# Performance work log

Hardware: AMD Instinct MI355X
Metric: run time of the kernel (lower is better)

The kernel has to match this reference:

```python
import jax, jax.numpy as jnp
import numpy as np

B, C, H, W = 64, 2048, 14, 14
HID, OUT = 2048, 256
NUM_HEADS = 8
SCALE = 1.0
BN_EPS = 1e-5
NORM_EPS = 1e-12


def setup_inputs() -> dict:
    key = jax.random.key(0)
    ks = jax.random.split(key, 5)
    inp = {
        "x": jax.random.normal(ks[0], (B, C, H, W), dtype=jnp.float32),
        # proj MLP1D: conv1(k=1) -> BN -> ReLU -> conv2(k=1), bias=False
        "w1_p": jax.random.normal(ks[1], (HID, C), dtype=jnp.float32) * 0.02,
        "g_p": jnp.ones((HID,), dtype=jnp.float32),
        "b_p": jnp.zeros((HID,), dtype=jnp.float32),
        "w2_p": jax.random.normal(ks[2], (OUT, HID), dtype=jnp.float32) * 0.02,
        # proj_obj MLP1D (same structure)
        "w1_o": jax.random.normal(ks[3], (HID, C), dtype=jnp.float32) * 0.02,
        "g_o": jnp.ones((HID,), dtype=jnp.float32),
        "b_o": jnp.zeros((HID,), dtype=jnp.float32),
        "w2_o": jax.random.normal(ks[4], (OUT, HID), dtype=jnp.float32) * 0.02,
    }
    return inp


def _mlp1d(x, w1, gamma, beta, w2):
    # x: [b, c_in, L]; 1x1 conv == channel matmul
    h = jnp.einsum('oc,bcl->bol', w1, x)  # [b, HID, L]
    # BatchNorm1d, training mode: stats over (batch, length) per channel
    mu = jnp.mean(h, axis=(0, 2), keepdims=True)
    var = jnp.mean(jnp.square(h - mu), axis=(0, 2), keepdims=True)
    h = (h - mu) * jax.lax.rsqrt(var + BN_EPS)
    h = h * gamma[None, :, None] + beta[None, :, None]
    h = jax.nn.relu(h)
    return jnp.einsum('oc,bcl->bol', w2, h)  # [b, OUT, L]


def reference(x, w1_p, g_p, b_p, w2_p, w1_o, g_o, b_o, w2_o):
    b, c, h, w = x.shape
    L = h * w
    xf = x.reshape(b, c, L)                       # [b, c, L]
    x_pool = jnp.mean(xf, axis=2, keepdims=True)  # adaptive_avg_pool2d(1)
    z = _mlp1d(jnp.concatenate([x_pool, xf], axis=2), w1_p, g_p, b_p, w2_p)  # [b, OUT, L+1]
    z_g = z[:, :, :1]          # [b, OUT, 1]
    z_feat = z[:, :, 1:]       # [b, OUT, L]
    # L2 normalize over channel dim, then scale
    nrm = jnp.sqrt(jnp.sum(jnp.square(z_feat), axis=1, keepdims=True))
    a = z_feat / jnp.maximum(nrm, NORM_EPS) / SCALE
    a = a.reshape(b, NUM_HEADS, -1, L)            # [b, H, K, L], K = OUT/H
    obj_attn_raw = jax.nn.softmax(a, axis=-1)
    obj_attn = obj_attn_raw                        # group branch: same softmax
    xh = xf.reshape(b, NUM_HEADS, c // NUM_HEADS, L)
    # matmul(x, attn^T): [b,H,Ch,L] x [b,H,K,L] -> [b,H,Ch,K]
    obj_val = jnp.einsum('bhcl,bhkl->bhck', xh, obj_attn)
    obj_val = obj_val.reshape(b, c, obj_attn.shape[2])  # [b, c, K]
    obj_val = _mlp1d(obj_val, w1_o, g_o, b_o, w2_o)      # [b, OUT, K]
    return (z_g, obj_val, obj_attn, obj_attn_raw)
```

## Files before the change

kernel.cpp:

```cpp
#include <hip/hip_runtime.h>
#include <hip/hip_bf16.h>
#include <math.h>

typedef __bf16 bf16;
typedef bf16 bf16x8 __attribute__((ext_vector_type(8)));
typedef float f32x4 __attribute__((ext_vector_type(4)));

constexpr int BATCH = 64;
constexpr int CIN   = 2048;
constexpr int HIDN  = 2048;
constexpr int OUTN  = 256;
constexpr int LL    = 196;
constexpr int LCAT  = 197;
constexpr int P1V   = BATCH * LCAT;
constexpr int P1P   = 12672;
constexpr size_t O_ZG   = 0;
constexpr size_t O_OVAL = (size_t)BATCH * OUTN;
constexpr size_t O_ATT  = O_OVAL + (size_t)BATCH * OUTN * 32;
constexpr size_t O_ATTR = O_ATT + (size_t)BATCH * OUTN * LL;

constexpr size_t WS_XCAT = 0;
constexpr size_t WS_V2   = WS_XCAT;
constexpr size_t WS_H2T  = WS_XCAT + (size_t)(16u<<20);
constexpr size_t WS_PART = WS_XCAT + (size_t)(28u<<20);
constexpr size_t WS_HT   = 51904512;
constexpr size_t WS_Z    = WS_HT + 51904512;
constexpr size_t WS_W1B  = WS_Z + 12976128;
constexpr size_t WS_W2B  = WS_W1B + 8388608;
constexpr size_t WS_W1OB = WS_W2B + 1048576;
constexpr size_t WS_W2OB = WS_W1OB + 8388608;
constexpr size_t WS_NRM  = WS_W2OB + 1048576;
constexpr size_t WS_SC1  = WS_NRM + 50176;
constexpr size_t WS_SH1  = WS_SC1 + 8192;
constexpr size_t WS_SC2  = WS_SH1 + 8192;
constexpr size_t WS_SH2  = WS_SC2 + 8192;

__device__ __forceinline__ void gload16(const bf16* g, bf16* l){
  __builtin_amdgcn_global_load_lds((const __attribute__((address_space(1))) void*)g,
                                   (__attribute__((address_space(3))) void*)l, 16, 0, 0);
}

__global__ __launch_bounds__(256) void cast_k(const float* __restrict__ s, bf16* __restrict__ d, int n){
  int i = blockIdx.x * 256 + threadIdx.x;
  if (i < n) d[i] = (bf16)s[i];
}
__global__ __launch_bounds__(256) void zero_b16(bf16* p, int n){
  int i = blockIdx.x * 256 + threadIdx.x;
  if (i < n) p[i] = (bf16)0.f;
}

__global__ __launch_bounds__(256) void prep_k(const float* __restrict__ x, bf16* __restrict__ xcat){
  __shared__ float xs[64][201];
  int b  = blockIdx.x >> 5;
  int cg = blockIdx.x & 31;
  int c0 = cg * 64;
  int t  = threadIdx.x;
  const float* xb = x + ((size_t)b * CIN + c0) * LL;
  #pragma unroll
  for (int i = 0; i < 16; i++){
    int idx = i * 256 + t;
    int cc = idx >> 6, q = idx & 63;
    if (q < 49){
      float4 v = *(const float4*)(xb + (size_t)cc * LL + q * 4);
      xs[cc][q*4+0] = v.x; xs[cc][q*4+1] = v.y; xs[cc][q*4+2] = v.z; xs[cc][q*4+3] = v.w;
    }
  }
  __syncthreads();
  if (t < 64){
    float s = 0.f;
    for (int l = 0; l < LL; l++) s += xs[t][l];
    xcat[(size_t)(b * LCAT) * CIN + c0 + t] = (bf16)(s * (1.f / (float)LL));
  }
  int lw = t >> 3, cg8 = t & 7;
  #pragma unroll
  for (int pass = 0; pass < 7; pass++){
    int l = pass * 32 + lw;
    if (l < LL){
      bf16x8 w;
      #pragma unroll
      for (int j = 0; j < 8; j++) w[j] = (bf16)xs[cg8 * 8 + j][l];
      *(bf16x8*)(xcat + (size_t)(b * LCAT + 1 + l) * CIN + c0 + cg8 * 8) = w;
    }
  }
}

__global__ __launch_bounds__(256) void stats_part_k(const bf16* __restrict__ src, int rows, int rpg,
                                                    float* __restrict__ part){
  int o  = threadIdx.x * 8;
  int r0 = blockIdx.x * rpg;
  int r1 = min(rows, r0 + rpg);
  float s[8] = {0.f,0.f,0.f,0.f,0.f,0.f,0.f,0.f};
  float q[8] = {0.f,0.f,0.f,0.f,0.f,0.f,0.f,0.f};
  for (int r = r0; r < r1; r++){
    bf16x8 v = *(const bf16x8*)(src + (size_t)r * 2048 + o);
    #pragma unroll
    for (int j = 0; j < 8; j++){ float f = (float)v[j]; s[j] += f; q[j] += f * f; }
  }
  float* p = part + (size_t)blockIdx.x * 4096;
  #pragma unroll
  for (int j = 0; j < 8; j++){ p[o + j] = s[j]; p[2048 + o + j] = q[j]; }
}

__global__ __launch_bounds__(256) void finalize_k(const float* __restrict__ part, int np,
                                                  const float* __restrict__ g, const float* __restrict__ b,
                                                  float n, float* __restrict__ scale, float* __restrict__ shift){
  int o = blockIdx.x * 256 + threadIdx.x;
  float s = 0.f, q = 0.f;
  for (int p = 0; p < np; p++){
    s += part[(size_t)p * 4096 + o];
    q += part[(size_t)p * 4096 + 2048 + o];
  }
  float mu  = s / n;
  float var = q / n - mu * mu;
  float sc  = g[o] / sqrtf(var + 1e-5f);
  scale[o] = sc;
  shift[o] = b[o] - mu * sc;
}

__global__ __launch_bounds__(256) void zg_k(const float* __restrict__ z, float* __restrict__ dout){
  int gidx = blockIdx.x * 256 + threadIdx.x;
  int b = gidx >> 8, c = gidx & 255;
  dout[O_ZG + gidx] = z[(size_t)c * P1P + b * LCAT];
}

__global__ __launch_bounds__(256) void nrm_k(const float* __restrict__ z, float* __restrict__ nrm){
  int b = blockIdx.x, t = threadIdx.x;
  if (t >= LL) return;
  float acc = 0.f;
  const float* zb = z + (size_t)b * LCAT + 1 + t;
  for (int c = 0; c < OUTN; c++){
    float v = zb[(size_t)c * P1P];
    acc += v * v;
  }
  nrm[b * LL + t] = sqrtf(acc);
}

__global__ __launch_bounds__(64) void softmax_k(const float* __restrict__ z, const float* __restrict__ nrm,
                                                float* __restrict__ dout){
  int bc = blockIdx.x;
  int b  = bc >> 8;
  int lane = threadIdx.x;
  const float* zr = z + (size_t)(bc & 255) * P1P + b * LCAT + 1;
  const float* nr = nrm + b * LL;
  float a[4];
  float mx = -1e30f;
  #pragma unroll
  for (int j = 0; j < 4; j++){
    int l = lane + j * 64;
    if (l < LL){
      float v = zr[l] / fmaxf(nr[l], 1e-12f);
      a[j] = v; mx = fmaxf(mx, v);
    } else a[j] = -1e30f;
  }
  #pragma unroll
  for (int s = 1; s < 64; s <<= 1) mx = fmaxf(mx, __shfl_xor(mx, s, 64));
  float sum = 0.f;
  #pragma unroll
  for (int j = 0; j < 4; j++){
    a[j] = (a[j] > -1e29f) ? expf(a[j] - mx) : 0.f;
    sum += a[j];
  }
  #pragma unroll
  for (int s = 1; s < 64; s <<= 1) sum += __shfl_xor(sum, s, 64);
  float inv = 1.f / sum;
  float* o1 = dout + O_ATT  + (size_t)bc * LL;
  float* o2 = dout + O_ATTR + (size_t)bc * LL;
  #pragma unroll
  for (int j = 0; j < 4; j++){
    int l = lane + j * 64;
    if (l < LL){ float r = a[j] * inv; o1[l] = r; o2[l] = r; }
  }
}

template<int CFG>
__global__ __launch_bounds__(256)
void gemm_k(const void* __restrict__ Ap, const void* __restrict__ Qp, void* __restrict__ Cp,
            const float* __restrict__ sc, const float* __restrict__ sh)
{
  constexpr int BM  = (CFG==5) ? 32 : (CFG==4 ? 64 : 128);
  constexpr int BN  = (CFG==5) ? 256 : (CFG==4 ? 64 : 128);
  constexpr int WR  = (CFG==5) ? 1 : 2;
  constexpr int WC  = 4 / WR;
  constexpr int WTM = BM / WR, WTN = BN / WC;
  constexpr int FM  = WTM / 16, FN = WTN / 16;
  constexpr int KT  = (CFG==5) ? 4 : 32;
  constexpr bool F32S = (CFG==5);
  constexpr bool QBN  = (CFG==2) || (CFG==4);
  constexpr bool AGL  = !F32S;
  constexpr bool QGL  = (CFG==1) || (CFG==3);
  constexpr int LDA = F32S ? LL : 2048;
  constexpr int LDQ = F32S ? LL : 2048;
  constexpr int CA  = BM / 32;
  constexpr int CQ  = BN / 32;

  __shared__ bf16 Ps[BM * 64];
  __shared__ bf16 Qs[BN * 64];

  const int t = threadIdx.x;
  const int lane = t & 63;
  const int wid  = t >> 6;
  const int wr = wid / WC, wc = wid % WC;
  const int sw8 = ((lane & 7) ^ (lane >> 3)) * 8;

  size_t aBase = 0, qBase = 0;
  int mOff = 0, nOff = 0;
  if constexpr (CFG == 5){
    int bh = blockIdx.x;
    aBase = (size_t)bh * 32 * LL;
    qBase = ((size_t)(bh >> 3) * 2048 + (size_t)(bh & 7) * 256) * LL;
    mOff = (bh >> 3) * 32;
    nOff = (bh & 7) * 256;
  } else if constexpr (CFG == 1){
    int bid = blockIdx.x;
    int wg = (bid & 7) * 198 + (bid >> 3);
    mOff = (wg >> 4) * BM;  nOff = (wg & 15) * BN;
    aBase = (size_t)mOff * LDA; qBase = (size_t)nOff * LDQ;
  } else if constexpr (CFG == 3){
    int bid = blockIdx.x;
    int wg = (bid & 7) * 32 + (bid >> 3);
    mOff = (wg >> 4) * BM;  nOff = (wg & 15) * BN;
    aBase = (size_t)mOff * LDA; qBase = (size_t)nOff * LDQ;
  } else {
    mOff = blockIdx.x * BM;
    nOff = blockIdx.y * BN;
    aBase = (size_t)mOff * LDA;
    qBase = (size_t)nOff * LDQ;
  }

  f32x4 acc[FM][FN] = {};

  for (int kt = 0; kt < KT; ++kt){
    const int k0 = kt * 64;
    bf16x8 ra[CA], rq[CQ];
    if constexpr (!AGL){
      #pragma unroll
      for (int i = 0; i < CA; i++){
        int ch = i * 256 + t;
        int row = ch >> 3, kc = ch & 7, kg = k0 + kc * 8;
        const float* g = (const float*)Ap + aBase + (size_t)row * LDA + kg;
        #pragma unroll
        for (int jj = 0; jj < 8; jj += 4){
          if (kg + jj + 3 < LL){
            float4 v = *(const float4*)(g + jj);
            ra[i][jj] = (bf16)v.x; ra[i][jj+1] = (bf16)v.y;
            ra[i][jj+2] = (bf16)v.z; ra[i][jj+3] = (bf16)v.w;
          } else {
            for (int j = jj; j < jj + 4; j++) ra[i][j] = (bf16)((kg + j) < LL ? g[j] : 0.f);
          }
        }
      }
    }
    if constexpr (!QGL){
      #pragma unroll
      for (int i = 0; i < CQ; i++){
        int ch = i * 256 + t;
        int row = ch >> 3, kc = ch & 7, kg = k0 + kc * 8;
        if constexpr (F32S){
          const float* g = (const float*)Qp + qBase + (size_t)row * LDQ + kg;
          #pragma unroll
          for (int jj = 0; jj < 8; jj += 4){
            if (kg + jj + 3 < LL){
              float4 v = *(const float4*)(g + jj);
              rq[i][jj] = (bf16)v.x; rq[i][jj+1] = (bf16)v.y;
              rq[i][jj+2] = (bf16)v.z; rq[i][jj+3] = (bf16)v.w;
            } else {
              for (int j = jj; j < jj + 4; j++) rq[i][j] = (bf16)((kg + j) < LL ? g[j] : 0.f);
            }
          }
        } else {
          bf16x8 raw = *(const bf16x8*)((const bf16*)Qp + qBase + (size_t)row * LDQ + kg);
          #pragma unroll
          for (int j = 0; j < 8; j++){
            float f = (float)raw[j] * sc[kg + j] + sh[kg + j];
            rq[i][j] = (bf16)fmaxf(f, 0.f);
          }
        }
      }
    }
    __syncthreads();
    if constexpr (AGL){
      #pragma unroll
      for (int c = 0; c < CA; c++){
        int chunk = wid * CA + c;
        int row = chunk * 8 + (lane >> 3);
        gload16((const bf16*)Ap + aBase + (size_t)row * LDA + k0 + sw8, &Ps[chunk * 512]);
      }
    }
    if constexpr (QGL){
      #pragma unroll
      for (int c = 0; c < CQ; c++){
        int chunk = wid * CQ + c;
        int row = chunk * 8 + (lane >> 3);
        gload16((const bf16*)Qp + qBase + (size_t)row * LDQ + k0 + sw8, &Qs[chunk * 512]);
      }
    }
    if constexpr (!AGL){
      #pragma unroll
      for (int i = 0; i < CA; i++){
        int ch = i * 256 + t; int row = ch >> 3, kc = ch & 7;
        *(bf16x8*)&Ps[row * 64 + ((kc ^ (row & 7)) << 3)] = ra[i];
      }
    }
    if constexpr (!QGL){
      #pragma unroll
      for (int i = 0; i < CQ; i++){
        int ch = i * 256 + t; int row = ch >> 3, kc = ch & 7;
        *(bf16x8*)&Qs[row * 64 + ((kc ^ (row & 7)) << 3)] = rq[i];
      }
    }
    __syncthreads();
    #pragma unroll
    for (int ks = 0; ks < 2; ++ks){
      const int kcl = ks * 4 + (lane >> 4);
      bf16x8 af[FM], qf[FN];
      #pragma unroll
      for (int m = 0; m < FM; m++){
        int row = wr * WTM + m * 16 + (lane & 15);
        af[m] = *(const bf16x8*)&Ps[row * 64 + ((kcl ^ (row & 7)) << 3)];
      }
      #pragma unroll
      for (int n = 0; n < FN; n++){
        int row = wc * WTN + n * 16 + (lane & 15);
        qf[n] = *(const bf16x8*)&Qs[row * 64 + ((kcl ^ (row & 7)) << 3)];
      }
      #pragma unroll
      for (int m = 0; m < FM; m++)
        #pragma unroll
        for (int n = 0; n < FN; n++)
          acc[m][n] = __builtin_amdgcn_mfma_f32_16x16x32_bf16(af[m], qf[n], acc[m][n], 0, 0, 0);
    }
  }

  #pragma unroll
  for (int m = 0; m < FM; m++){
    #pragma unroll
    for (int n = 0; n < FN; n++){
      #pragma unroll
      for (int r = 0; r < 4; r++){
        int row = mOff + wr * WTM + m * 16 + (lane >> 4) * 4 + r;
        int col = nOff + wc * WTN + n * 16 + (lane & 15);
        float v = acc[m][n][r];
        if constexpr (CFG == 1 || CFG == 3 || CFG == 5){
          ((bf16*)Cp)[(size_t)row * 2048 + col] = (bf16)v;
        } else if constexpr (CFG == 2){
          ((float*)Cp)[(size_t)row * P1P + col] = v;
        } else {
          ((float*)Cp)[O_OVAL + (size_t)(col >> 5) * 8192 + (size_t)row * 32 + (col & 31)] = v;
        }
      }
    }
  }
}

extern "C" void kernel_launch(void* const* d_in, const int* in_sizes, int n_in,
                              void* d_out, int out_size, void* d_ws, size_t ws_size,
                              hipStream_t stream){
  const float* x   = (const float*)d_in[0];
  const float* w1p = (const float*)d_in[1];
  const float* gp  = (const float*)d_in[2];
  const float* bp  = (const float*)d_in[3];
  const float* w2p = (const float*)d_in[4];
  const float* w1o = (const float*)d_in[5];
  const float* go  = (const float*)d_in[6];
  const float* bo  = (const float*)d_in[7];
  const float* w2o = (const float*)d_in[8];
  float* out = (float*)d_out;
  char* ws = (char*)d_ws;

  bf16* xcat = (bf16*)(ws + WS_XCAT);
  bf16* v2   = (bf16*)(ws + WS_V2);
  bf16* h2t  = (bf16*)(ws + WS_H2T);
  float* part = (float*)(ws + WS_PART);
  bf16* hT   = (bf16*)(ws + WS_HT);
  float* z   = (float*)(ws + WS_Z);
  bf16* w1b  = (bf16*)(ws + WS_W1B);
  bf16* w2b  = (bf16*)(ws + WS_W2B);
  bf16* w1ob = (bf16*)(ws + WS_W1OB);
  bf16* w2ob = (bf16*)(ws + WS_W2OB);
  float* nrmw = (float*)(ws + WS_NRM);
  float* sc1 = (float*)(ws + WS_SC1);
  float* sh1 = (float*)(ws + WS_SH1);
  float* sc2 = (float*)(ws + WS_SC2);
  float* sh2 = (float*)(ws + WS_SH2);

  cast_k<<<16384, 256, 0, stream>>>(w1p, w1b, HIDN * CIN);
  cast_k<<<2048,  256, 0, stream>>>(w2p, w2b, OUTN * HIDN);
  cast_k<<<16384, 256, 0, stream>>>(w1o, w1ob, HIDN * CIN);
  cast_k<<<2048,  256, 0, stream>>>(w2o, w2ob, OUTN * HIDN);
  zero_b16<<<512, 256, 0, stream>>>(xcat + (size_t)P1V * 2048, (P1P - P1V) * 2048);
  prep_k<<<2048, 256, 0, stream>>>(x, xcat);

  gemm_k<1><<<1584, 256, 0, stream>>>(xcat, w1b, hT, nullptr, nullptr);
  stats_part_k<<<256, 256, 0, stream>>>(hT, P1V, 50, part);
  finalize_k<<<8, 256, 0, stream>>>(part, 256, gp, bp, (float)P1V, sc1, sh1);
  gemm_k<2><<<dim3(2, 99), 256, 0, stream>>>(w2b, hT, z, sc1, sh1);

  zg_k<<<64, 256, 0, stream>>>(z, out);
  nrm_k<<<64, 256, 0, stream>>>(z, nrmw);
  softmax_k<<<16384, 64, 0, stream>>>(z, nrmw, out);

  gemm_k<5><<<512, 256, 0, stream>>>(out + O_ATT, x, v2, nullptr, nullptr);
  gemm_k<3><<<256, 256, 0, stream>>>(v2, w1ob, h2t, nullptr, nullptr);
  stats_part_k<<<64, 256, 0, stream>>>(h2t, 2048, 32, part);
  finalize_k<<<8, 256, 0, stream>>>(part, 64, go, bo, 2048.f, sc2, sh2);
  gemm_k<4><<<dim3(4, 32), 256, 0, stream>>>(w2ob, h2t, out, sc2, sh2);
}
```

Before: 673.2 us.

## Replace first projection GEMM with 256x256-tile, 8-wave, double-buffered ping-pong kernel

Swaps the generic 128x128 GEMM for the big projection (12.6K x 2048 x 2048) for a dedicated 512-thread kernel with 256x256 tiles. It uses double-buffered LDS filled by direct global-to-LDS loads and interleaves MFMA quads with barriers and s_setprio so that loads overlap compute. The aim is more data reuse per tile and fewer stalls in the dominant GEMM. The M padding grows to a multiple of 256, which adds some wasted rows and shifts the workspace offsets, and the large LDS footprint limits occupancy.

```diff
diff --git a/kernel.cpp b/kernel.cpp
--- a/kernel.cpp
+++ b/kernel.cpp
@@ -13,7 +13,7 @@
 constexpr int LL    = 196;
 constexpr int LCAT  = 197;
 constexpr int P1V   = BATCH * LCAT;
-constexpr int P1P   = 12672;
+constexpr int P1P   = 12800;
 constexpr size_t O_ZG   = 0;
 constexpr size_t O_OVAL = (size_t)BATCH * OUTN;
 constexpr size_t O_ATT  = O_OVAL + (size_t)BATCH * OUTN * 32;
@@ -23,21 +23,26 @@
 constexpr size_t WS_V2   = WS_XCAT;
 constexpr size_t WS_H2T  = WS_XCAT + (size_t)(16u<<20);
 constexpr size_t WS_PART = WS_XCAT + (size_t)(28u<<20);
-constexpr size_t WS_HT   = 51904512;
-constexpr size_t WS_Z    = WS_HT + 51904512;
-constexpr size_t WS_W1B  = WS_Z + 12976128;
-constexpr size_t WS_W2B  = WS_W1B + 8388608;
-constexpr size_t WS_W1OB = WS_W2B + 1048576;
-constexpr size_t WS_W2OB = WS_W1OB + 8388608;
-constexpr size_t WS_NRM  = WS_W2OB + 1048576;
-constexpr size_t WS_SC1  = WS_NRM + 50176;
-constexpr size_t WS_SH1  = WS_SC1 + 8192;
-constexpr size_t WS_SC2  = WS_SH1 + 8192;
-constexpr size_t WS_SH2  = WS_SC2 + 8192;
+constexpr size_t WS_HT   = 52428800;
+constexpr size_t WS_Z    = 104857600;
+constexpr size_t WS_W1B  = 117964800;
+constexpr size_t WS_W2B  = 126353408;
+constexpr size_t WS_W1OB = 127401984;
+constexpr size_t WS_W2OB = 135790592;
+constexpr size_t WS_NRM  = 136839168;
+constexpr size_t WS_SC1  = 136889344;
+constexpr size_t WS_SH1  = 136897536;
+constexpr size_t WS_SC2  = 136905728;
+constexpr size_t WS_SH2  = 136913920;
 
 __device__ __forceinline__ void gload16(const bf16* g, bf16* l){
   __builtin_amdgcn_global_load_lds((const __attribute__((address_space(1))) void*)g,
                                    (__attribute__((address_space(3))) void*)l, 16, 0, 0);
+}
+__device__ __forceinline__ void wgb(){
+  asm volatile("" ::: "memory");
+  __builtin_amdgcn_s_barrier();
+  asm volatile("" ::: "memory");
 }
 
 __global__ __launch_bounds__(256) void cast_k(const float* __restrict__ s, bf16* __restrict__ d, int n){
@@ -172,10 +177,115 @@
   }
 }
 
+
+template<int MBASE, int NB>
+__device__ __forceinline__ void mfma_quad(const bf16x8 (&af)[2][4], const bf16x8 (&bf)[2][2],
+                                          f32x4 (&acc)[8][4]){
+  __builtin_amdgcn_s_setprio(1);
+  #pragma unroll
+  for (int ks = 0; ks < 2; ks++)
+    #pragma unroll
+    for (int j = 0; j < 4; j++)
+      #pragma unroll
+      for (int jj = 0; jj < 2; jj++)
+        acc[MBASE+j][NB+jj] = __builtin_amdgcn_mfma_f32_16x16x32_bf16(af[ks][j], bf[ks][jj],
+                                                                      acc[MBASE+j][NB+jj], 0, 0, 0);
+  __builtin_amdgcn_s_setprio(0);
+}
+template<int MSET>
+__device__ __forceinline__ void read_afr(const bf16* Ab, int wr, const int (&offk)[2], bf16x8 (&af)[2][4]){
+  #pragma unroll
+  for (int ks = 0; ks < 2; ks++)
+    #pragma unroll
+    for (int j = 0; j < 4; j++)
+      af[ks][j] = *(const bf16x8*)(Ab + (wr*128 + (MSET*4+j)*16)*64 + offk[ks]);
+}
+template<int NB>
+__device__ __forceinline__ void read_bfr(const bf16* Bb, int wc, const int (&offk)[2], bf16x8 (&bf)[2][2]){
+  #pragma unroll
+  for (int ks = 0; ks < 2; ks++)
+    #pragma unroll
+    for (int jj = 0; jj < 2; jj++)
+      bf[ks][jj] = *(const bf16x8*)(Bb + (wc*64 + (NB+jj)*16)*64 + offk[ks]);
+}
+
+__global__ __launch_bounds__(512, 2)
+void gemm1_k(const bf16* __restrict__ A, const bf16* __restrict__ B, bf16* __restrict__ C){
+  constexpr int ATI = 256 * 64;
+  __shared__ bf16 As[2 * ATI];
+  __shared__ bf16 Bs[2 * ATI];
+  const int t = threadIdx.x, lane = t & 63, wid = t >> 6;
+  const int wr = wid >> 2, wc = wid & 3;
+  const int sw8 = ((lane & 7) ^ (lane >> 3)) * 8;
+  int bid = blockIdx.x;
+  int wg  = (bid & 7) * 50 + (bid >> 3);
+  const int mOff = (wg >> 3) * 256, nOff = (wg & 7) * 256;
+  int offk[2];
+  #pragma unroll
+  for (int ks = 0; ks < 2; ks++) offk[ks] = (lane & 15) * 64 + (((ks*4 + (lane >> 4)) ^ (lane & 7)) << 3);
+
+  f32x4 acc[8][4] = {};
+  bf16x8 afr0[2][4], afr1[2][4], bfr0[2][2], bfr1[2][2];
+
+  auto stage = [&](const bf16* __restrict__ G, int rbase, bf16* lds, int kt, int h){
+    #pragma unroll
+    for (int c = 0; c < 2; c++){
+      int chunk = h * 16 + wid * 2 + c;
+      int row = chunk * 8 + (lane >> 3);
+      gload16(G + (size_t)(rbase + row) * 2048 + kt * 64 + sw8, lds + chunk * 512);
+    }
+  };
+
+  stage(A, mOff, As, 0, 0);        stage(A, mOff, As, 0, 1);
+  stage(B, nOff, Bs, 0, 0);        stage(B, nOff, Bs, 0, 1);
+  stage(A, mOff, As + ATI, 1, 0);  stage(A, mOff, As + ATI, 1, 1);
+  asm volatile("s_waitcnt vmcnt(4)" ::: "memory");
+  wgb();
+
+  for (int i = 0; i < 16; i++){
+    const int te = 2*i, to = 2*i + 1;
+    const bool PRE = (i < 15);
+    read_afr<0>(As, wr, offk, afr0);  read_bfr<0>(Bs, wc, offk, bfr0);
+    stage(B, nOff, Bs + ATI, to, 0);
+    wgb();  mfma_quad<0,0>(afr0, bfr0, acc);  wgb();
+    read_afr<1>(As, wr, offk, afr1);
+    stage(B, nOff, Bs + ATI, to, 1);
+    wgb();  mfma_quad<4,0>(afr1, bfr0, acc);  wgb();
+    read_bfr<2>(Bs, wc, offk, bfr1);
+    if (PRE) stage(A, mOff, As, te + 2, 0);
+    wgb();  mfma_quad<4,2>(afr1, bfr1, acc);  wgb();
+    if (PRE){ stage(A, mOff, As, te + 2, 1); asm volatile("s_waitcnt vmcnt(4)" ::: "memory"); }
+    else    { asm volatile("s_waitcnt vmcnt(0)" ::: "memory"); }
+    wgb();  mfma_quad<0,2>(afr0, bfr1, acc);  wgb();
+    read_afr<0>(As + ATI, wr, offk, afr0);  read_bfr<0>(Bs + ATI, wc, offk, bfr0);
+    if (PRE) stage(B, nOff, Bs, te + 2, 0);
+    wgb();  mfma_quad<0,0>(afr0, bfr0, acc);  wgb();
+    read_afr<1>(As + ATI, wr, offk, afr1);
+    if (PRE) stage(B, nOff, Bs, te + 2, 1);
+    wgb();  mfma_quad<4,0>(afr1, bfr0, acc);  wgb();
+    read_bfr<2>(Bs + ATI, wc, offk, bfr1);
+    if (PRE) stage(A, mOff, As + ATI, to + 2, 0);
+    wgb();  mfma_quad<4,2>(afr1, bfr1, acc);  wgb();
+    if (PRE){ stage(A, mOff, As + ATI, to + 2, 1); asm volatile("s_waitcnt vmcnt(4)" ::: "memory"); }
+    wgb();  mfma_quad<0,2>(afr0, bfr1, acc);  wgb();
+  }
+
+  #pragma unroll
+  for (int m = 0; m < 8; m++)
+    #pragma unroll
+    for (int n = 0; n < 4; n++)
+      #pragma unroll
+      for (int r = 0; r < 4; r++){
+        int row = mOff + wr*128 + m*16 + (lane >> 4)*4 + r;
+        int col = nOff + wc*64  + n*16 + (lane & 15);
+        C[(size_t)row * 2048 + col] = (bf16)acc[m][n][r];
+      }
+}
+
 template<int CFG>
-__global__ __launch_bounds__(256)
-void gemm_k(const void* __restrict__ Ap, const void* __restrict__ Qp, void* __restrict__ Cp,
-            const float* __restrict__ sc, const float* __restrict__ sh)
+__device__ __forceinline__
+void gemm_body(const void* __restrict__ Ap, const void* __restrict__ Qp, void* __restrict__ Cp,
+               const float* __restrict__ sc, const float* __restrict__ sh)
 {
   constexpr int BM  = (CFG==5) ? 32 : (CFG==4 ? 64 : 128);
   constexpr int BN  = (CFG==5) ? 256 : (CFG==4 ? 64 : 128);
@@ -187,7 +297,7 @@
   constexpr bool F32S = (CFG==5);
   constexpr bool QBN  = (CFG==2) || (CFG==4);
   constexpr bool AGL  = !F32S;
-  constexpr bool QGL  = (CFG==1) || (CFG==3);
+  constexpr bool QGL  = (CFG==3);
   constexpr int LDA = F32S ? LL : 2048;
   constexpr int LDQ = F32S ? LL : 2048;
   constexpr int CA  = BM / 32;
@@ -210,11 +320,6 @@
     qBase = ((size_t)(bh >> 3) * 2048 + (size_t)(bh & 7) * 256) * LL;
     mOff = (bh >> 3) * 32;
     nOff = (bh & 7) * 256;
-  } else if constexpr (CFG == 1){
-    int bid = blockIdx.x;
-    int wg = (bid & 7) * 198 + (bid >> 3);
-    mOff = (wg >> 4) * BM;  nOff = (wg & 15) * BN;
-    aBase = (size_t)mOff * LDA; qBase = (size_t)nOff * LDQ;
   } else if constexpr (CFG == 3){
     int bid = blockIdx.x;
     int wg = (bid & 7) * 32 + (bid >> 3);
@@ -340,7 +445,7 @@
         int row = mOff + wr * WTM + m * 16 + (lane >> 4) * 4 + r;
         int col = nOff + wc * WTN + n * 16 + (lane & 15);
         float v = acc[m][n][r];
-        if constexpr (CFG == 1 || CFG == 3 || CFG == 5){
+        if constexpr (CFG == 3 || CFG == 5){
           ((bf16*)Cp)[(size_t)row * 2048 + col] = (bf16)v;
         } else if constexpr (CFG == 2){
           ((float*)Cp)[(size_t)row * P1P + col] = v;
@@ -351,6 +456,15 @@
     }
   }
 }
+
+__global__ __launch_bounds__(256) void gemm2_k(const void* A, const void* Q, void* C,
+                                               const float* sc, const float* sh){ gemm_body<2>(A,Q,C,sc,sh); }
+__global__ __launch_bounds__(256) void gemm3_k(const void* A, const void* Q, void* C,
+                                               const float* sc, const float* sh){ gemm_body<3>(A,Q,C,sc,sh); }
+__global__ __launch_bounds__(256) void gemm4_k(const void* A, const void* Q, void* C,
+                                               const float* sc, const float* sh){ gemm_body<4>(A,Q,C,sc,sh); }
+__global__ __launch_bounds__(256) void gemm5_k(const void* A, const void* Q, void* C,
+                                               const float* sc, const float* sh){ gemm_body<5>(A,Q,C,sc,sh); }
 
 extern "C" void kernel_launch(void* const* d_in, const int* in_sizes, int n_in,
                               void* d_out, int out_size, void* d_ws, size_t ws_size,
@@ -387,21 +501,21 @@
   cast_k<<<2048,  256, 0, stream>>>(w2p, w2b, OUTN * HIDN);
   cast_k<<<16384, 256, 0, stream>>>(w1o, w1ob, HIDN * CIN);
   cast_k<<<2048,  256, 0, stream>>>(w2o, w2ob, OUTN * HIDN);
-  zero_b16<<<512, 256, 0, stream>>>(xcat + (size_t)P1V * 2048, (P1P - P1V) * 2048);
+  zero_b16<<<1536, 256, 0, stream>>>(xcat + (size_t)P1V * 2048, (P1P - P1V) * 2048);
   prep_k<<<2048, 256, 0, stream>>>(x, xcat);
 
-  gemm_k<1><<<1584, 256, 0, stream>>>(xcat, w1b, hT, nullptr, nullptr);
+  gemm1_k<<<400, 512, 0, stream>>>(xcat, w1b, hT);
   stats_part_k<<<256, 256, 0, stream>>>(hT, P1V, 50, part);
   finalize_k<<<8, 256, 0, stream>>>(part, 256, gp, bp, (float)P1V, sc1, sh1);
-  gemm_k<2><<<dim3(2, 99), 256, 0, stream>>>(w2b, hT, z, sc1, sh1);
+  gemm2_k<<<dim3(2, 100), 256, 0, stream>>>(w2b, hT, z, sc1, sh1);
 
   zg_k<<<64, 256, 0, stream>>>(z, out);
   nrm_k<<<64, 256, 0, stream>>>(z, nrmw);
   softmax_k<<<16384, 64, 0, stream>>>(z, nrmw, out);
 
-  gemm_k<5><<<512, 256, 0, stream>>>(out + O_ATT, x, v2, nullptr, nullptr);
-  gemm_k<3><<<256, 256, 0, stream>>>(v2, w1ob, h2t, nullptr, nullptr);
+  gemm5_k<<<512, 256, 0, stream>>>(out + O_ATT, x, v2, nullptr, nullptr);
+  gemm3_k<<<256, 256, 0, stream>>>(v2, w1ob, h2t, nullptr, nullptr);
   stats_part_k<<<64, 256, 0, stream>>>(h2t, 2048, 32, part);
   finalize_k<<<8, 256, 0, stream>>>(part, 64, go, bo, 2048.f, sc2, sh2);
-  gemm_k<4><<<dim3(4, 32), 256, 0, stream>>>(w2ob, h2t, out, sc2, sh2);
-}
+  gemm4_k<<<dim3(4, 32), 256, 0, stream>>>(w2ob, h2t, out, sc2, sh2);
+}
```

Result: faster. 656.6 us (-2.5%).
